# Kernel optimization log

Measured on AMD Instinct MI355X. Metric: run time of the kernel, lower is better.

The kernel has to match this reference:

```python
import jax, jax.numpy as jnp
import numpy as np

B, S, D, H, HS = 2, 2048, 1024, 16, 64


def setup_inputs() -> dict:
    key = jax.random.key(0)
    ks = jax.random.split(key, 4)
    x = jax.random.normal(ks[0], (B, S, D), dtype=jnp.float32)
    # causal mask: 1.0 where key_pos <= query_pos, else 0.0
    mask = jnp.tril(jnp.ones((S, S), dtype=jnp.float32))
    w_qkv = jax.random.normal(ks[1], (D, 3, H, HS), dtype=jnp.float32) * 0.02
    b_qkv = jnp.zeros((3, H, HS), dtype=jnp.float32)
    w_proj = jax.random.normal(ks[2], (H, HS, D), dtype=jnp.float32) * 0.02
    b_proj = jnp.zeros((D,), dtype=jnp.float32)
    return {"x": x, "mask": mask, "w_qkv": w_qkv, "b_qkv": b_qkv,
            "w_proj": w_proj, "b_proj": b_proj}


def reference(x, mask, w_qkv, b_qkv, w_proj, b_proj):
    # c_attn: [B,S,D] @ [D,3,H,HS] -> [B,S,3,H,HS]
    qkv = jnp.einsum('bsd,dthc->bsthc', x, w_qkv) + b_qkv
    q, k, v = qkv[:, :, 0], qkv[:, :, 1], qkv[:, :, 2]  # [B,S,H,HS]
    scale = jax.lax.rsqrt(float(HS))
    q = q * scale
    # scores over head_size: [B,H,S(query),S(key)]
    scores = jnp.einsum('bqhc,bkhc->bhqk', q, k)
    scores = scores + (1.0 - mask) * -1e9
    weights = jax.nn.softmax(scores, axis=-1).astype(x.dtype)
    # attn_pdrop = 0.0 / inference: dropout is identity
    attn = jnp.einsum('bhqk,bkhc->bqhc', weights, v)  # [B,S,H,HS]
    out = jnp.einsum('bqhc,hcd->bqd', attn, w_proj) + b_proj
    return out
```

## Files before the change

### kernel.cpp

```cpp
#include <hip/hip_runtime.h>
#include <hip/hip_bf16.h>


#define Bb 2
#define Ss 2048
#define Dd 1024
#define Hh 16
#define HSs 64

typedef __bf16 bf16x8 __attribute__((ext_vector_type(8)));
typedef float  f32x4  __attribute__((ext_vector_type(4)));

__device__ __forceinline__ unsigned short f2bf(float f) {
  unsigned int u = __float_as_uint(f);
  unsigned int lsb = (u >> 16) & 1u;
  u += 0x7fffu + lsb;
  return (unsigned short)(u >> 16);
}

__device__ __forceinline__ void async16(const unsigned short* g, unsigned short* l) {
  __builtin_amdgcn_global_load_lds(
      (const __attribute__((address_space(1))) unsigned int*)g,
      (__attribute__((address_space(3))) unsigned int*)l,
      16, 0, 0);
}

__global__ __launch_bounds__(256) void k_cvt_bf16(const float* __restrict__ in,
                                                  unsigned short* __restrict__ out,
                                                  int n) {
  int i = (blockIdx.x * 256 + threadIdx.x) * 4;
  int stride = gridDim.x * 256 * 4;
  for (; i < n; i += stride) {
    float4 v = *reinterpret_cast<const float4*>(in + i);
    ushort4 o;
    o.x = f2bf(v.x); o.y = f2bf(v.y); o.z = f2bf(v.z); o.w = f2bf(v.w);
    *reinterpret_cast<ushort4*>(out + i) = o;
  }
}

__global__ __launch_bounds__(256) void k_transpose_bf16(const float* __restrict__ in,
                                                        unsigned short* __restrict__ out,
                                                        int R, int C) {
  __shared__ float t[32][33];
  int c0 = blockIdx.x * 32, r0 = blockIdx.y * 32;
  int tx = threadIdx.x, ty = threadIdx.y;
  #pragma unroll
  for (int i = 0; i < 32; i += 8)
    t[ty + i][tx] = in[(size_t)(r0 + ty + i) * C + (c0 + tx)];
  __syncthreads();
  #pragma unroll
  for (int i = 0; i < 32; i += 8)
    out[(size_t)(c0 + ty + i) * R + (r0 + tx)] = f2bf(t[tx][ty + i]);
}

__global__ __launch_bounds__(256) void k_gemm_qkv(const unsigned short* __restrict__ A,
                                                  const unsigned short* __restrict__ Bt,
                                                  const float* __restrict__ bias,
                                                  unsigned short* __restrict__ Qg,
                                                  unsigned short* __restrict__ Kg,
                                                  unsigned short* __restrict__ Vt) {
  __shared__ unsigned short As[128 * 64];
  __shared__ unsigned short Bs[128 * 64];
  const int K = 1024;
  int bid = blockIdx.x;
  int swz = (bid % 8) * 96 + bid / 8;
  int tm = swz / 24, tn = swz % 24;
  int m0 = tm * 128, n0 = tn * 128;
  int tid = threadIdx.x;
  int w = tid >> 6, l = tid & 63;
  int lr = l & 15, lg = l >> 4;
  int wm = (w >> 1) * 64, wn = (w & 1) * 64;
  int srow = l >> 3, scol = (l & 7) * 8;

  f32x4 acc[4][4];
  #pragma unroll
  for (int i = 0; i < 4; ++i)
    #pragma unroll
    for (int j = 0; j < 4; ++j)
      acc[i][j] = (f32x4){0.f, 0.f, 0.f, 0.f};

  for (int k0 = 0; k0 < K; k0 += 64) {
    #pragma unroll
    for (int c = 0; c < 4; ++c) {
      int chunk = w * 4 + c;
      int row = chunk * 8 + srow;
      async16(&A[(size_t)(m0 + row) * K + k0 + scol], &As[chunk * 512]);
      async16(&Bt[(size_t)(n0 + row) * K + k0 + scol], &Bs[chunk * 512]);
    }
    __syncthreads();
    #pragma unroll
    for (int kk = 0; kk < 64; kk += 32) {
      bf16x8 af[4], bfr[4];
      #pragma unroll
      for (int mf = 0; mf < 4; ++mf)
        af[mf] = *reinterpret_cast<const bf16x8*>(&As[(wm + mf * 16 + lr) * 64 + kk + lg * 8]);
      #pragma unroll
      for (int nf = 0; nf < 4; ++nf)
        bfr[nf] = *reinterpret_cast<const bf16x8*>(&Bs[(wn + nf * 16 + lr) * 64 + kk + lg * 8]);
      #pragma unroll
      for (int mf = 0; mf < 4; ++mf)
        #pragma unroll
        for (int nf = 0; nf < 4; ++nf)
          acc[mf][nf] = __builtin_amdgcn_mfma_f32_16x16x32_bf16(af[mf], bfr[nf], acc[mf][nf], 0, 0, 0);
    }
    __syncthreads();
  }

  #pragma unroll
  for (int mf = 0; mf < 4; ++mf) {
    #pragma unroll
    for (int nf = 0; nf < 4; ++nf) {
      int n = n0 + wn + nf * 16 + lr;
      int t = n >> 10, r = n & 1023;
      int h = r >> 6, cc = r & 63;
      float bv = bias[n];
      if (t == 2) {
        int m = m0 + wm + mf * 16 + lg * 4;
        int b = m >> 11, s = m & 2047;
        ushort4 pk;
        pk.x = f2bf(acc[mf][nf][0] + bv);
        pk.y = f2bf(acc[mf][nf][1] + bv);
        pk.z = f2bf(acc[mf][nf][2] + bv);
        pk.w = f2bf(acc[mf][nf][3] + bv);
        *reinterpret_cast<ushort4*>(&Vt[((size_t)(b * Hh + h) * HSs + cc) * Ss + s]) = pk;
      } else {
        #pragma unroll
        for (int j = 0; j < 4; ++j) {
          int m = m0 + wm + mf * 16 + lg * 4 + j;
          int b = m >> 11, s = m & 2047;
          size_t idx = ((size_t)(b * Hh + h) * Ss + s) * HSs + cc;
          float v = acc[mf][nf][j] + bv;
          if (t == 0) Qg[idx] = f2bf(v * 0.125f);
          else        Kg[idx] = f2bf(v);
        }
      }
    }
  }
}

__global__ __launch_bounds__(512, 4) void k_attn(const unsigned short* __restrict__ Qg,
                                                 const unsigned short* __restrict__ Kg,
                                                 const unsigned short* __restrict__ Vt,
                                                 unsigned short* __restrict__ Ob) {
  __shared__ unsigned short Ks[2][64 * 64];
  __shared__ unsigned short Vs[2][64 * 64];
  __shared__ unsigned short Ps[8][16 * 72];

  int bid = blockIdx.x;
  int p  = bid >> 5;
  int bh = bid & 31;
  int b = bh >> 4, h = bh & 15;

  int tid = threadIdx.x;
  int w = tid >> 6, l = tid & 63;
  int g = w >> 2;
  int myqt = g ? (31 - p) : p;
  int qs0 = myqt * 64;
  int lr = l & 15, lg = l >> 4;
  int qw = qs0 + (w & 3) * 16;
  int srow = l >> 3, scol = (l & 7) * 8;
  int swcol = scol ^ (srow << 3);

  bf16x8 qf[2];
  #pragma unroll
  for (int kx = 0; kx < 2; ++kx)
    qf[kx] = *reinterpret_cast<const bf16x8*>(
        &Qg[((size_t)bh * Ss + qw + lr) * HSs + kx * 32 + lg * 8]);

  f32x4 oacc[4];
  #pragma unroll
  for (int nf = 0; nf < 4; ++nf) oacc[nf] = (f32x4){0.f, 0.f, 0.f, 0.f};
  float mrun[4], lrun[4];
  #pragma unroll
  for (int j = 0; j < 4; ++j) { mrun[j] = -1e30f; lrun[j] = 0.f; }

  int ntiles = 32 - p;
  {
    int row = w * 8 + srow;
    async16(&Kg[((size_t)bh * Ss + 0 * 64 + row) * HSs + swcol], &Ks[0][w * 512]);
    async16(&Vt[((size_t)bh * HSs + row) * Ss + 0 * 64 + swcol], &Vs[0][w * 512]);
  }
  __syncthreads();

  for (int t = 0; t < ntiles; ++t) {
    int cur = t & 1;
    if (t + 1 < ntiles) {
      int row = w * 8 + srow;
      async16(&Kg[((size_t)bh * Ss + (t + 1) * 64 + row) * HSs + swcol], &Ks[cur ^ 1][w * 512]);
      async16(&Vt[((size_t)bh * HSs + row) * Ss + (t + 1) * 64 + swcol], &Vs[cur ^ 1][w * 512]);
    }

    if (t <= myqt) {
      f32x4 sacc[4];
      #pragma unroll
      for (int nf = 0; nf < 4; ++nf) sacc[nf] = (f32x4){0.f, 0.f, 0.f, 0.f};
      #pragma unroll
      for (int kx = 0; kx < 2; ++kx) {
        bf16x8 kf[4];
        #pragma unroll
        for (int nf = 0; nf < 4; ++nf)
          kf[nf] = *reinterpret_cast<const bf16x8*>(
              &Ks[cur][(nf * 16 + lr) * 64 + ((kx * 32 + lg * 8) ^ ((lr & 7) << 3))]);
        #pragma unroll
        for (int nf = 0; nf < 4; ++nf)
          sacc[nf] = __builtin_amdgcn_mfma_f32_16x16x32_bf16(qf[kx], kf[nf], sacc[nf], 0, 0, 0);
      }

      if (t == myqt) {
        #pragma unroll
        for (int nf = 0; nf < 4; ++nf) {
          int kcol = qs0 + nf * 16 + lr;
          #pragma unroll
          for (int j = 0; j < 4; ++j) {
            int qg2 = qw + lg * 4 + j;
            if (kcol > qg2) sacc[nf][j] = -1e30f;
          }
        }
      }

      #pragma unroll
      for (int j = 0; j < 4; ++j) {
        float rmax = fmaxf(fmaxf(sacc[0][j], sacc[1][j]), fmaxf(sacc[2][j], sacc[3][j]));
        #pragma unroll
        for (int d = 1; d < 16; d <<= 1)
          rmax = fmaxf(rmax, __shfl_xor(rmax, d));
        float mnew = fmaxf(mrun[j], rmax);
        float cf = __expf(mrun[j] - mnew);
        mrun[j] = mnew;
        float psum = 0.f;
        #pragma unroll
        for (int nf = 0; nf < 4; ++nf) {
          float pv = __expf(sacc[nf][j] - mnew);
          sacc[nf][j] = pv;
          psum += pv;
        }
        #pragma unroll
        for (int d = 1; d < 16; d <<= 1)
          psum += __shfl_xor(psum, d);
        lrun[j] = lrun[j] * cf + psum;
        #pragma unroll
        for (int nf = 0; nf < 4; ++nf)
          oacc[nf][j] *= cf;
      }

      #pragma unroll
      for (int nf = 0; nf < 4; ++nf)
        #pragma unroll
        for (int j = 0; j < 4; ++j)
          Ps[w][(lg * 4 + j) * 72 + nf * 16 + lr] = f2bf(sacc[nf][j]);

      #pragma unroll
      for (int kx = 0; kx < 2; ++kx) {
        bf16x8 pf = *reinterpret_cast<const bf16x8*>(&Ps[w][lr * 72 + kx * 32 + lg * 8]);
        bf16x8 vf[4];
        #pragma unroll
        for (int nf = 0; nf < 4; ++nf)
          vf[nf] = *reinterpret_cast<const bf16x8*>(
              &Vs[cur][(nf * 16 + lr) * 64 + ((kx * 32 + lg * 8) ^ ((lr & 7) << 3))]);
        #pragma unroll
        for (int nf = 0; nf < 4; ++nf)
          oacc[nf] = __builtin_amdgcn_mfma_f32_16x16x32_bf16(pf, vf[nf], oacc[nf], 0, 0, 0);
      }
    }
    __syncthreads();
  }

  #pragma unroll
  for (int j = 0; j < 4; ++j) {
    float rinv = 1.0f / lrun[j];
    int s = qw + lg * 4 + j;
    #pragma unroll
    for (int nf = 0; nf < 4; ++nf) {
      int c = nf * 16 + lr;
      Ob[((size_t)(b * Ss + s)) * Dd + h * HSs + c] = f2bf(oacc[nf][j] * rinv);
    }
  }
}

__global__ __launch_bounds__(256) void k_gemm_out(const unsigned short* __restrict__ A,
                                                  const unsigned short* __restrict__ Bt,
                                                  const float* __restrict__ bias,
                                                  float* __restrict__ Out) {
  __shared__ unsigned short As[128 * 64];
  __shared__ unsigned short Bs[128 * 64];
  const int K = 1024;
  int bid = blockIdx.x;
  int swz = (bid % 8) * 32 + bid / 8;
  int tm = swz / 8, tn = swz % 8;
  int m0 = tm * 128, n0 = tn * 128;
  int tid = threadIdx.x;
  int w = tid >> 6, l = tid & 63;
  int lr = l & 15, lg = l >> 4;
  int wm = (w >> 1) * 64, wn = (w & 1) * 64;
  int srow = l >> 3, scol = (l & 7) * 8;

  f32x4 acc[4][4];
  #pragma unroll
  for (int i = 0; i < 4; ++i)
    #pragma unroll
    for (int j = 0; j < 4; ++j)
      acc[i][j] = (f32x4){0.f, 0.f, 0.f, 0.f};

  for (int k0 = 0; k0 < K; k0 += 64) {
    #pragma unroll
    for (int c = 0; c < 4; ++c) {
      int chunk = w * 4 + c;
      int row = chunk * 8 + srow;
      async16(&A[(size_t)(m0 + row) * K + k0 + scol], &As[chunk * 512]);
      async16(&Bt[(size_t)(n0 + row) * K + k0 + scol], &Bs[chunk * 512]);
    }
    __syncthreads();
    #pragma unroll
    for (int kk = 0; kk < 64; kk += 32) {
      bf16x8 af[4], bfr[4];
      #pragma unroll
      for (int mf = 0; mf < 4; ++mf)
        af[mf] = *reinterpret_cast<const bf16x8*>(&As[(wm + mf * 16 + lr) * 64 + kk + lg * 8]);
      #pragma unroll
      for (int nf = 0; nf < 4; ++nf)
        bfr[nf] = *reinterpret_cast<const bf16x8*>(&Bs[(wn + nf * 16 + lr) * 64 + kk + lg * 8]);
      #pragma unroll
      for (int mf = 0; mf < 4; ++mf)
        #pragma unroll
        for (int nf = 0; nf < 4; ++nf)
          acc[mf][nf] = __builtin_amdgcn_mfma_f32_16x16x32_bf16(af[mf], bfr[nf], acc[mf][nf], 0, 0, 0);
    }
    __syncthreads();
  }

  #pragma unroll
  for (int mf = 0; mf < 4; ++mf)
    #pragma unroll
    for (int nf = 0; nf < 4; ++nf) {
      int n = n0 + wn + nf * 16 + lr;
      float bv = bias[n];
      #pragma unroll
      for (int j = 0; j < 4; ++j) {
        int m = m0 + wm + mf * 16 + lg * 4 + j;
        Out[(size_t)m * 1024 + n] = acc[mf][nf][j] + bv;
      }
    }
}

extern "C" void kernel_launch(void* const* d_in, const int* in_sizes, int n_in,
                              void* d_out, int out_size, void* d_ws, size_t ws_size,
                              hipStream_t stream) {
  (void)in_sizes; (void)n_in; (void)out_size; (void)ws_size;
  const float* x      = (const float*)d_in[0];
  const float* w_qkv  = (const float*)d_in[2];
  const float* b_qkv  = (const float*)d_in[3];
  const float* w_proj = (const float*)d_in[4];
  const float* b_proj = (const float*)d_in[5];
  float* out = (float*)d_out;

  char* ws = (char*)d_ws;
  unsigned short* xb    = (unsigned short*)(ws);
  unsigned short* wqkvT = (unsigned short*)(ws + 8388608);
  unsigned short* wpT   = (unsigned short*)(ws + 14680064);
  unsigned short* Qg    = (unsigned short*)(ws + 16777216);
  unsigned short* Kg    = (unsigned short*)(ws + 25165824);
  unsigned short* Vt    = (unsigned short*)(ws + 33554432);
  unsigned short* attnb = (unsigned short*)(ws + 41943040);

  k_cvt_bf16<<<dim3(2048), dim3(256), 0, stream>>>(x, xb, Bb * Ss * Dd);
  k_transpose_bf16<<<dim3(96, 32), dim3(32, 8), 0, stream>>>(w_qkv, wqkvT, 1024, 3072);
  k_transpose_bf16<<<dim3(32, 32), dim3(32, 8), 0, stream>>>(w_proj, wpT, 1024, 1024);
  k_gemm_qkv<<<dim3(32 * 24), dim3(256), 0, stream>>>(xb, wqkvT, b_qkv, Qg, Kg, Vt);
  k_attn<<<dim3(512), dim3(512), 0, stream>>>(Qg, Kg, Vt, attnb);
  k_gemm_out<<<dim3(32 * 8), dim3(256), 0, stream>>>(attnb, wpT, b_proj, out);
}
```

Measured before the change: 237.1 us.

## Rework attention kernel: 128-row query tiles, exp2 softmax with lazy rescale, setprio

The attention kernel now gives each block one contiguous 128-row query tile, paired as Q and 15-Q across block indices for causal load balance, instead of two 64-row tiles from opposite ends. Per-wave causal skipping and masking are computed from each wave's own rows. The softmax folds log2(e) into the Q scale so it can use exp2f, and it rescales the running max and accumulators only when some row max grows by more than 8 (log2 units), which skips most rescale multiplies. s_setprio hints are placed around the MFMA sections. Lazy rescaling allows unnormalised values up to 2^8 in the accumulators and bf16 P, a small precision risk, and the new tiling changes block scheduling balance.

```diff
diff --git a/kernel.cpp b/kernel.cpp
--- a/kernel.cpp
+++ b/kernel.cpp
@@ -130,7 +130,7 @@
           int b = m >> 11, s = m & 2047;
           size_t idx = ((size_t)(b * Hh + h) * Ss + s) * HSs + cc;
           float v = acc[mf][nf][j] + bv;
-          if (t == 0) Qg[idx] = f2bf(v * 0.125f);
+          if (t == 0) Qg[idx] = f2bf(v * 0.1803368801111244f);
           else        Kg[idx] = f2bf(v);
         }
       }
@@ -147,19 +147,18 @@
   __shared__ unsigned short Ps[8][16 * 72];
 
   int bid = blockIdx.x;
-  int p  = bid >> 5;
-  int bh = bid & 31;
+  int pi = bid >> 5, bh = bid & 31;
+  int Q = (pi < 8) ? pi : 23 - pi;
   int b = bh >> 4, h = bh & 15;
+  int qs0 = Q * 128;
 
   int tid = threadIdx.x;
   int w = tid >> 6, l = tid & 63;
-  int g = w >> 2;
-  int myqt = g ? (31 - p) : p;
-  int qs0 = myqt * 64;
   int lr = l & 15, lg = l >> 4;
-  int qw = qs0 + (w & 3) * 16;
+  int qw = qs0 + w * 16;
   int srow = l >> 3, scol = (l & 7) * 8;
   int swcol = scol ^ (srow << 3);
+  int row = w * 8 + srow;
 
   bf16x8 qf[2];
   #pragma unroll
@@ -174,26 +173,23 @@
   #pragma unroll
   for (int j = 0; j < 4; ++j) { mrun[j] = -1e30f; lrun[j] = 0.f; }
 
-  int ntiles = 32 - p;
-  {
-    int row = w * 8 + srow;
-    async16(&Kg[((size_t)bh * Ss + 0 * 64 + row) * HSs + swcol], &Ks[0][w * 512]);
-    async16(&Vt[((size_t)bh * HSs + row) * Ss + 0 * 64 + swcol], &Vs[0][w * 512]);
-  }
+  int ntiles = 2 * Q + 2;
+  async16(&Kg[((size_t)bh * Ss + row) * HSs + swcol], &Ks[0][w * 512]);
+  async16(&Vt[((size_t)bh * HSs + row) * Ss + swcol], &Vs[0][w * 512]);
   __syncthreads();
 
   for (int t = 0; t < ntiles; ++t) {
     int cur = t & 1;
     if (t + 1 < ntiles) {
-      int row = w * 8 + srow;
       async16(&Kg[((size_t)bh * Ss + (t + 1) * 64 + row) * HSs + swcol], &Ks[cur ^ 1][w * 512]);
       async16(&Vt[((size_t)bh * HSs + row) * Ss + (t + 1) * 64 + swcol], &Vs[cur ^ 1][w * 512]);
     }
 
-    if (t <= myqt) {
+    if (t * 64 <= qw + 15) {
       f32x4 sacc[4];
       #pragma unroll
       for (int nf = 0; nf < 4; ++nf) sacc[nf] = (f32x4){0.f, 0.f, 0.f, 0.f};
+      __builtin_amdgcn_s_setprio(1);
       #pragma unroll
       for (int kx = 0; kx < 2; ++kx) {
         bf16x8 kf[4];
@@ -205,11 +201,12 @@
         for (int nf = 0; nf < 4; ++nf)
           sacc[nf] = __builtin_amdgcn_mfma_f32_16x16x32_bf16(qf[kx], kf[nf], sacc[nf], 0, 0, 0);
       }
-
-      if (t == myqt) {
+      __builtin_amdgcn_s_setprio(0);
+
+      if (t * 64 + 63 > qw) {
         #pragma unroll
         for (int nf = 0; nf < 4; ++nf) {
-          int kcol = qs0 + nf * 16 + lr;
+          int kcol = t * 64 + nf * 16 + lr;
           #pragma unroll
           for (int j = 0; j < 4; ++j) {
             int qg2 = qw + lg * 4 + j;
@@ -218,29 +215,42 @@
         }
       }
 
+      float rmax[4];
       #pragma unroll
       for (int j = 0; j < 4; ++j) {
-        float rmax = fmaxf(fmaxf(sacc[0][j], sacc[1][j]), fmaxf(sacc[2][j], sacc[3][j]));
+        float rm = fmaxf(fmaxf(sacc[0][j], sacc[1][j]), fmaxf(sacc[2][j], sacc[3][j]));
         #pragma unroll
         for (int d = 1; d < 16; d <<= 1)
-          rmax = fmaxf(rmax, __shfl_xor(rmax, d));
-        float mnew = fmaxf(mrun[j], rmax);
-        float cf = __expf(mrun[j] - mnew);
-        mrun[j] = mnew;
+          rm = fmaxf(rm, __shfl_xor(rm, d));
+        rmax[j] = rm;
+      }
+      bool need = (rmax[0] > mrun[0] + 8.f) | (rmax[1] > mrun[1] + 8.f) |
+                  (rmax[2] > mrun[2] + 8.f) | (rmax[3] > mrun[3] + 8.f);
+      if (__any(need)) {
+        #pragma unroll
+        for (int j = 0; j < 4; ++j) {
+          float mnew = fmaxf(mrun[j], rmax[j]);
+          float cf = exp2f(mrun[j] - mnew);
+          mrun[j] = mnew;
+          lrun[j] *= cf;
+          #pragma unroll
+          for (int nf = 0; nf < 4; ++nf)
+            oacc[nf][j] *= cf;
+        }
+      }
+      #pragma unroll
+      for (int j = 0; j < 4; ++j) {
         float psum = 0.f;
         #pragma unroll
         for (int nf = 0; nf < 4; ++nf) {
-          float pv = __expf(sacc[nf][j] - mnew);
+          float pv = exp2f(sacc[nf][j] - mrun[j]);
           sacc[nf][j] = pv;
           psum += pv;
         }
         #pragma unroll
         for (int d = 1; d < 16; d <<= 1)
           psum += __shfl_xor(psum, d);
-        lrun[j] = lrun[j] * cf + psum;
-        #pragma unroll
-        for (int nf = 0; nf < 4; ++nf)
-          oacc[nf][j] *= cf;
+        lrun[j] += psum;
       }
 
       #pragma unroll
@@ -249,6 +259,7 @@
         for (int j = 0; j < 4; ++j)
           Ps[w][(lg * 4 + j) * 72 + nf * 16 + lr] = f2bf(sacc[nf][j]);
 
+      __builtin_amdgcn_s_setprio(1);
       #pragma unroll
       for (int kx = 0; kx < 2; ++kx) {
         bf16x8 pf = *reinterpret_cast<const bf16x8*>(&Ps[w][lr * 72 + kx * 32 + lg * 8]);
@@ -261,6 +272,7 @@
         for (int nf = 0; nf < 4; ++nf)
           oacc[nf] = __builtin_amdgcn_mfma_f32_16x16x32_bf16(pf, vf[nf], oacc[nf], 0, 0, 0);
       }
+      __builtin_amdgcn_s_setprio(0);
     }
     __syncthreads();
   }
```

Result: slower. 250.8 us (+5.8%).
